# Optimization experiments

Measured on AMD Instinct MI355X. Metric: run time of the kernel, lower is better.

## Reference

```python
import jax, jax.numpy as jnp
import numpy as np

N_TYPES = 4
N_RELS = 8
N, E, IN_DIM, OUT_DIM = 100000, 1600000, 64, 64
SQRT_DK = float(np.sqrt(OUT_DIM))  # num_heads = 1 -> d_k = out_dim


def setup_inputs() -> dict:
    key = jax.random.key(0)
    ks = jax.random.split(key, 12)
    s = 0.05  # keep activations well-scaled (xavier-ish)
    h = jax.random.normal(ks[0], (N, IN_DIM), jnp.float32)
    node_type = jax.random.randint(ks[1], (N,), 0, N_TYPES, jnp.int32)
    src = jax.random.randint(ks[2], (E,), 0, N, jnp.int32)
    dst = jax.random.randint(ks[3], (E,), 0, N, jnp.int32)
    etype = jax.random.randint(ks[4], (E,), 0, N_RELS, jnp.int32)
    k_lin = jax.random.normal(ks[5], (N_TYPES, IN_DIM, OUT_DIM), jnp.float32) * s
    q_lin = jax.random.normal(ks[6], (N_TYPES, IN_DIM, OUT_DIM), jnp.float32) * s
    v_lin = jax.random.normal(ks[7], (N_TYPES, IN_DIM, OUT_DIM), jnp.float32) * s
    a_lin = jax.random.normal(ks[8], (N_TYPES, OUT_DIM, OUT_DIM), jnp.float32) * s
    rel_att = jax.random.normal(ks[9], (N_RELS, OUT_DIM, OUT_DIM), jnp.float32) * s
    rel_msg = jax.random.normal(ks[10], (N_RELS, OUT_DIM, OUT_DIM), jnp.float32) * s
    rel_pri = jnp.ones((N_RELS,), jnp.float32)
    skip = jnp.ones((N_TYPES,), jnp.float32)
    return dict(h=h, node_type=node_type, src=src, dst=dst, etype=etype,
                k_lin=k_lin, q_lin=q_lin, v_lin=v_lin, a_lin=a_lin,
                rel_att=rel_att, rel_msg=rel_msg, rel_pri=rel_pri, skip=skip)


def _typed_matmul(x, W, node_type):
    # rgnn_relational_matmul_no_scatter_gather_list: per-node-type GEMM.
    # Small fixed loop over node types (4), masked accumulate.
    out = jnp.zeros((x.shape[0], W.shape[-1]), x.dtype)
    for t in range(W.shape[0]):
        out = out + jnp.where((node_type == t)[:, None], x @ W[t], 0.0)
    return out


def reference(h, node_type, src, dst, etype, k_lin, q_lin, v_lin, a_lin,
              rel_att, rel_msg, rel_pri, skip):
    # per-node-type K/Q/V projections (num_heads==1, d_k==out_dim)
    k = _typed_matmul(h, k_lin, node_type)  # [N, d_k]
    q = _typed_matmul(h, q_lin, node_type)  # [N, d_k]
    v = _typed_matmul(h, v_lin, node_type)  # [N, d_k]

    # q @ relation_att, computed per relation for ALL nodes then gathered per edge
    # (avoids materializing [E, d_k, d_k] relation weights per edge)
    qW = jnp.einsum('nd,rde->rne', q, rel_att)  # [R, N, d_k]
    t_edge = qW[etype, dst]                      # [E, d_k]  (dst-side product)
    # attention score: <q_dst @ W_att_r, k_src>
    score = jnp.sum(t_edge * k[src], axis=-1)    # [E]

    # edge softmax over incoming edges of each dst, scaled by pri/sqrt(d_k)
    logits = score * (rel_pri / SQRT_DK)[etype]
    m = jax.ops.segment_max(logits, dst, num_segments=N)
    ex = jnp.exp(logits - m[dst])
    den = jax.ops.segment_sum(ex, dst, num_segments=N)
    alpha = ex / jnp.where(den[dst] == 0, 1.0, den[dst])  # [E]

    # message: v_src @ W_msg_r, per relation then gathered per edge
    vW = jnp.einsum('nd,rde->rne', v, rel_msg)   # [R, N, d_k]
    msg = vW[etype, src]                          # [E, d_k]

    # softmax-weighted aggregation to dst nodes
    agg = jax.ops.segment_sum(alpha[:, None] * msg, dst, num_segments=N)  # [N, d_k]

    # output per-node-type GEMM with sigmoid(skip)-scaled a_linears
    W_out = jax.nn.sigmoid(skip)[:, None, None] * a_lin
    return _typed_matmul(agg, W_out, node_type)  # [N, out_dim]
```

## Files before the change

kernel.cpp:

```cpp
#include <hip/hip_runtime.h>
#include <math.h>

#define DIM 64
#define NT 4
#define NR 8

typedef __attribute__((ext_vector_type(8))) short bf16x8;
typedef __attribute__((ext_vector_type(8))) unsigned short u16x8;
typedef __attribute__((ext_vector_type(4))) float f32x4;

__device__ __forceinline__ unsigned short f2bf(float f) {
    unsigned u = __float_as_uint(f);
    return (unsigned short)((u + 0x7FFF + ((u >> 16) & 1)) >> 16);
}
__device__ __forceinline__ float bf2f(unsigned short u) {
    return __uint_as_float((unsigned)u << 16);
}
__device__ __forceinline__ bf16x8 ldb16(const unsigned short* p) {
    return *((const bf16x8*)p);
}

__global__ void type_count(const int* __restrict__ ntype, int* __restrict__ tm, int N) {
    int i = blockIdx.x * blockDim.x + threadIdx.x;
    int t = (i < N) ? ntype[i] : -1;
    int lane = threadIdx.x & 63;
    #pragma unroll
    for (int tt = 0; tt < NT; tt++) {
        unsigned long long m = __ballot(t == tt);
        int c = __popcll(m);
        if (c && lane == (__ffsll((long long)m) - 1)) atomicAdd(&tm[tt], c);
    }
}

__global__ void type_scan(int* __restrict__ tm) {
    if (threadIdx.x == 0 && blockIdx.x == 0) {
        int b = 0;
        for (int t = 0; t < NT; t++) { tm[4 + t] = b; b += ((tm[t] + 63) >> 6) << 6; }
        tm[12] = b;
    }
}

__global__ void type_scatter(const int* __restrict__ ntype, int* __restrict__ tm,
                             int* __restrict__ order, int N) {
    int i = blockIdx.x * blockDim.x + threadIdx.x;
    int t = (i < N) ? ntype[i] : -1;
    int lane = threadIdx.x & 63;
    #pragma unroll
    for (int tt = 0; tt < NT; tt++) {
        unsigned long long m = __ballot(t == tt);
        int c = __popcll(m);
        if (!c) continue;
        int ldr = __ffsll((long long)m) - 1;
        int base = 0;
        if (lane == ldr) base = atomicAdd(&tm[8 + tt], c);
        base = __shfl(base, ldr, 64);
        if (t == tt) {
            int rank = __popcll(m & ((1ull << lane) - 1ull));
            order[tm[4 + tt] + base + rank] = i;
        }
    }
}

__global__ void proj_typed(const float* __restrict__ h, const int* __restrict__ ntype,
                           const int* __restrict__ order, const int* __restrict__ tm,
                           const float* __restrict__ Wk, const float* __restrict__ Wq,
                           const float* __restrict__ Wv,
                           unsigned short* __restrict__ kvbf, unsigned short* __restrict__ qbf,
                           int N) {
    __shared__ float xs[64][68];
    __shared__ float wsm[64][64];
    int t  = threadIdx.x;
    int n0 = blockIdx.x * 64;
    if (n0 >= tm[12]) return;
    int first = order[n0];
    if (first < 0) return;
    int ty = ntype[first];

    #pragma unroll
    for (int i = 0; i < 4; i++) {
        int idx = t + 256 * i;
        int row = idx >> 4, c4 = idx & 15;
        int gn = order[n0 + row];
        float4 xv = make_float4(0.f, 0.f, 0.f, 0.f);
        if (gn >= 0) xv = ((const float4*)(h + (size_t)gn * DIM))[c4];
        ((float4*)&xs[row][0])[c4] = xv;
    }

    const float* Ws[3] = { Wk + (size_t)ty * DIM * DIM,
                           Wq + (size_t)ty * DIM * DIM,
                           Wv + (size_t)ty * DIM * DIM };
    unsigned short* Os[3] = { kvbf, qbf, kvbf + 64 };
    const size_t   st[3] = { 128, 64, 128 };

    int og  = t & 15;
    int ng4 = (t >> 4) * 4;
    int g[4];
    #pragma unroll
    for (int j = 0; j < 4; j++) g[j] = order[n0 + ng4 + j];

    for (int mm = 0; mm < 3; mm++) {
        const float4* wg = (const float4*)Ws[mm];
        float4* wl = (float4*)&wsm[0][0];
        __syncthreads();
        #pragma unroll
        for (int i = 0; i < 4; i++) wl[t + 256 * i] = wg[t + 256 * i];
        __syncthreads();
        float4 a[4];
        #pragma unroll
        for (int j = 0; j < 4; j++) a[j] = make_float4(0.f, 0.f, 0.f, 0.f);
        #pragma unroll 8
        for (int d = 0; d < DIM; d++) {
            float4 wv = ((const float4*)&wsm[d][0])[og];
            #pragma unroll
            for (int j = 0; j < 4; j++) {
                float xx = xs[ng4 + j][d];
                a[j].x = fmaf(xx, wv.x, a[j].x); a[j].y = fmaf(xx, wv.y, a[j].y);
                a[j].z = fmaf(xx, wv.z, a[j].z); a[j].w = fmaf(xx, wv.w, a[j].w);
            }
        }
        unsigned short* ob = Os[mm];
        #pragma unroll
        for (int j = 0; j < 4; j++)
            if (g[j] >= 0)
                ((ushort4*)(ob + (size_t)g[j] * st[mm]))[og] =
                    make_ushort4(f2bf(a[j].x), f2bf(a[j].y), f2bf(a[j].z), f2bf(a[j].w));
    }
}

__global__ void prep_w(const float* __restrict__ A, const float* __restrict__ Mw,
                       unsigned short* __restrict__ At, unsigned short* __restrict__ Mt) {
    int i = blockIdx.x * blockDim.x + threadIdx.x;
    if (i >= NR * DIM * DIM) return;
    int r = i >> 12;
    int idx = i & 4095;
    int n = idx >> 6;
    int k = idx & 63;
    At[i] = f2bf(A[(r << 12) + k * DIM + n]);
    Mt[i] = f2bf(Mw[(r << 12) + k * DIM + n]);
}

__global__ void hist8(const int* __restrict__ dst, const int* __restrict__ et,
                      int* __restrict__ cnt, int E) {
    int e = blockIdx.x * blockDim.x + threadIdx.x;
    if (e < E) atomicAdd(&cnt[dst[e] * NR + et[e]], 1);
}

__global__ void scan1(const int* __restrict__ cnt, int* __restrict__ off,
                      int* __restrict__ bsum, int M) {
    __shared__ int buf[1024];
    int tid = threadIdx.x;
    int i = blockIdx.x * 1024 + tid;
    int x = (i < M) ? cnt[i] : 0;
    buf[tid] = x;
    __syncthreads();
    for (int s = 1; s < 1024; s <<= 1) {
        int t = (tid >= s) ? buf[tid - s] : 0;
        __syncthreads();
        buf[tid] += t;
        __syncthreads();
    }
    if (i < M) off[i] = buf[tid] - x;
    if (tid == 1023) bsum[blockIdx.x] = buf[1023];
}

__global__ void scan2(int* __restrict__ bsum, int nb) {
    __shared__ int buf[1024];
    __shared__ int carry;
    int tid = threadIdx.x;
    if (tid == 0) carry = 0;
    __syncthreads();
    for (int base = 0; base < nb; base += 1024) {
        int i = base + tid;
        int x = (i < nb) ? bsum[i] : 0;
        buf[tid] = x;
        __syncthreads();
        for (int s = 1; s < 1024; s <<= 1) {
            int t = (tid >= s) ? buf[tid - s] : 0;
            __syncthreads();
            buf[tid] += t;
            __syncthreads();
        }
        if (i < nb) bsum[i] = carry + buf[tid] - x;
        __syncthreads();
        if (tid == 1023) carry += buf[1023];
        __syncthreads();
    }
}

__global__ void scan3(int* __restrict__ off, const int* __restrict__ bsum, int M, int E) {
    int i = blockIdx.x * 1024 + threadIdx.x;
    if (i < M) off[i] += bsum[blockIdx.x];
    if (i == 0) off[M] = E;
}

__global__ void scatter8(const int* __restrict__ src, const int* __restrict__ dst,
                         const int* __restrict__ et, const int* __restrict__ off,
                         int* __restrict__ cnt2, int* __restrict__ se, int E) {
    int e = blockIdx.x * blockDim.x + threadIdx.x;
    if (e >= E) return;
    int key = dst[e] * NR + et[e];
    int p = off[key] + atomicAdd(&cnt2[key], 1);
    se[p] = src[e];
}

__global__ void __launch_bounds__(256)
fused_edge(const unsigned short* __restrict__ qbf,
           const unsigned short* __restrict__ kvbf,
           const unsigned short* __restrict__ At,
           const unsigned short* __restrict__ Mt,
           const int* __restrict__ se, const int* __restrict__ off8,
           const float* __restrict__ rel_pri,
           float* __restrict__ agg, int N) {
    __shared__ __align__(16) float qw[4][16][68];
    __shared__ __align__(16) unsigned short pl[4][16][72];
    const int t    = threadIdx.x;
    const int wave = t >> 6;
    const int m    = t & 15;
    const int quad = (t >> 4) & 3;
    const int half = m >> 3;
    const int oct  = m & 7;
    const int n0   = blockIdx.x * 64 + wave * 16;
    if (n0 >= N) return;

    bf16x8 qa0 = {0,0,0,0,0,0,0,0}, qa1 = {0,0,0,0,0,0,0,0};
    {
        const int gn = n0 + m;
        if (gn < N) {
            const unsigned short* qp = qbf + ((size_t)gn << 6) + quad * 8;
            qa0 = *((const bf16x8*)qp);
            qa1 = *((const bf16x8*)(qp + 32));
        }
    }

    int ov[4];
    #pragma unroll
    for (int j = 0; j < 4; j++) {
        const int nj = n0 + quad * 4 + j;
        ov[j] = (m < 9 && nj < N) ? off8[nj * NR + m] : 0;
    }

    f32x4 u0 = {0.f,0.f,0.f,0.f}, u1 = u0, u2 = u0, u3 = u0;
    float d0 = 0.f, d1 = 0.f, d2 = 0.f, d3 = 0.f;

    for (int r = 0; r < NR; r++) {
        const unsigned short* Ar = At + ((size_t)r << 12);
        f32x4 c0 = {0.f,0.f,0.f,0.f}, c1 = c0, c2 = c0, c3 = c0;
        c0 = __builtin_amdgcn_mfma_f32_16x16x32_bf16(qa0, ldb16(Ar + (( 0 + m) << 6)      + quad * 8), c0, 0, 0, 0);
        c1 = __builtin_amdgcn_mfma_f32_16x16x32_bf16(qa0, ldb16(Ar + ((16 + m) << 6)      + quad * 8), c1, 0, 0, 0);
        c2 = __builtin_amdgcn_mfma_f32_16x16x32_bf16(qa0, ldb16(Ar + ((32 + m) << 6)      + quad * 8), c2, 0, 0, 0);
        c3 = __builtin_amdgcn_mfma_f32_16x16x32_bf16(qa0, ldb16(Ar + ((48 + m) << 6)      + quad * 8), c3, 0, 0, 0);
        c0 = __builtin_amdgcn_mfma_f32_16x16x32_bf16(qa1, ldb16(Ar + (( 0 + m) << 6) + 32 + quad * 8), c0, 0, 0, 0);
        c1 = __builtin_amdgcn_mfma_f32_16x16x32_bf16(qa1, ldb16(Ar + ((16 + m) << 6) + 32 + quad * 8), c1, 0, 0, 0);
        c2 = __builtin_amdgcn_mfma_f32_16x16x32_bf16(qa1, ldb16(Ar + ((32 + m) << 6) + 32 + quad * 8), c2, 0, 0, 0);
        c3 = __builtin_amdgcn_mfma_f32_16x16x32_bf16(qa1, ldb16(Ar + ((48 + m) << 6) + 32 + quad * 8), c3, 0, 0, 0);

        #pragma unroll
        for (int reg = 0; reg < 4; reg++) {
            float* qr = &qw[wave][quad * 4 + reg][m];
            qr[ 0] = c0[reg]; qr[16] = c1[reg]; qr[32] = c2[reg]; qr[48] = c3[reg];
        }
        asm volatile("s_waitcnt lgkmcnt(0)" ::: "memory");

        const float pri = rel_pri[r] * 0.125f;
        #pragma unroll
        for (int j = 0; j < 4; j++) {
            const int i0 = __shfl(ov[j], r, 16);
            const int i1 = __shfl(ov[j], r + 1, 16);
            float dd = 0.f;
            float4 pa = make_float4(0.f, 0.f, 0.f, 0.f);
            float4 pb = make_float4(0.f, 0.f, 0.f, 0.f);
            if (i0 < i1) {
                const float4 tva = *((const float4*)&qw[wave][quad * 4 + j][oct * 8]);
                const float4 tvb = *((const float4*)&qw[wave][quad * 4 + j][oct * 8 + 4]);
                auto edge2 = [&](int base) {
                    const int idx  = base + half;
                    const bool val = idx < i1;
                    const int s    = se[val ? idx : i0];
                    const unsigned short* kvp = kvbf + ((size_t)s << 7) + oct * 8;
                    const u16x8 k8 = *((const u16x8*)kvp);
                    const u16x8 v8 = *((const u16x8*)(kvp + 64));
                    float p  = bf2f(k8[0]) * tva.x + bf2f(k8[1]) * tva.y +
                               bf2f(k8[2]) * tva.z + bf2f(k8[3]) * tva.w;
                    float p2 = bf2f(k8[4]) * tvb.x + bf2f(k8[5]) * tvb.y +
                               bf2f(k8[6]) * tvb.z + bf2f(k8[7]) * tvb.w;
                    p += p2;
                    p += __shfl_xor(p, 1, 16);
                    p += __shfl_xor(p, 2, 16);
                    p += __shfl_xor(p, 4, 16);
                    const float e = val ? __expf(p * pri) : 0.f;
                    dd += e;
                    pa.x = fmaf(e, bf2f(v8[0]), pa.x);
                    pa.y = fmaf(e, bf2f(v8[1]), pa.y);
                    pa.z = fmaf(e, bf2f(v8[2]), pa.z);
                    pa.w = fmaf(e, bf2f(v8[3]), pa.w);
                    pb.x = fmaf(e, bf2f(v8[4]), pb.x);
                    pb.y = fmaf(e, bf2f(v8[5]), pb.y);
                    pb.z = fmaf(e, bf2f(v8[6]), pb.z);
                    pb.w = fmaf(e, bf2f(v8[7]), pb.w);
                };
                int i = i0;
                for (; i + 2 < i1; i += 4) { edge2(i); edge2(i + 2); }
                for (; i < i1; i += 2) edge2(i);
                dd  += __shfl_xor(dd, 8, 16);
                pa.x += __shfl_xor(pa.x, 8, 16);
                pa.y += __shfl_xor(pa.y, 8, 16);
                pa.z += __shfl_xor(pa.z, 8, 16);
                pa.w += __shfl_xor(pa.w, 8, 16);
                pb.x += __shfl_xor(pb.x, 8, 16);
                pb.y += __shfl_xor(pb.y, 8, 16);
                pb.z += __shfl_xor(pb.z, 8, 16);
                pb.w += __shfl_xor(pb.w, 8, 16);
            }
            if (m < 8) {
                u16x8 w;
                w[0] = f2bf(pa.x); w[1] = f2bf(pa.y); w[2] = f2bf(pa.z); w[3] = f2bf(pa.w);
                w[4] = f2bf(pb.x); w[5] = f2bf(pb.y); w[6] = f2bf(pb.z); w[7] = f2bf(pb.w);
                *((u16x8*)&pl[wave][quad * 4 + j][m * 8]) = w;
            }
            if      (j == 0) d0 += dd;
            else if (j == 1) d1 += dd;
            else if (j == 2) d2 += dd;
            else             d3 += dd;
        }
        asm volatile("s_waitcnt lgkmcnt(0)" ::: "memory");

        const unsigned short* Mr = Mt + ((size_t)r << 12);
        const bf16x8 pa0 = *((const bf16x8*)&pl[wave][m][quad * 8]);
        const bf16x8 pa1 = *((const bf16x8*)&pl[wave][m][32 + quad * 8]);
        u0 = __builtin_amdgcn_mfma_f32_16x16x32_bf16(pa0, ldb16(Mr + (( 0 + m) << 6)      + quad * 8), u0, 0, 0, 0);
        u1 = __builtin_amdgcn_mfma_f32_16x16x32_bf16(pa0, ldb16(Mr + ((16 + m) << 6)      + quad * 8), u1, 0, 0, 0);
        u2 = __builtin_amdgcn_mfma_f32_16x16x32_bf16(pa0, ldb16(Mr + ((32 + m) << 6)      + quad * 8), u2, 0, 0, 0);
        u3 = __builtin_amdgcn_mfma_f32_16x16x32_bf16(pa0, ldb16(Mr + ((48 + m) << 6)      + quad * 8), u3, 0, 0, 0);
        u0 = __builtin_amdgcn_mfma_f32_16x16x32_bf16(pa1, ldb16(Mr + (( 0 + m) << 6) + 32 + quad * 8), u0, 0, 0, 0);
        u1 = __builtin_amdgcn_mfma_f32_16x16x32_bf16(pa1, ldb16(Mr + ((16 + m) << 6) + 32 + quad * 8), u1, 0, 0, 0);
        u2 = __builtin_amdgcn_mfma_f32_16x16x32_bf16(pa1, ldb16(Mr + ((32 + m) << 6) + 32 + quad * 8), u2, 0, 0, 0);
        u3 = __builtin_amdgcn_mfma_f32_16x16x32_bf16(pa1, ldb16(Mr + ((48 + m) << 6) + 32 + quad * 8), u3, 0, 0, 0);
        asm volatile("s_waitcnt lgkmcnt(0)" ::: "memory");
    }

    #pragma unroll
    for (int reg = 0; reg < 4; reg++) {
        const int n = n0 + quad * 4 + reg;
        if (n >= N) continue;
        const float dv  = (reg == 0) ? d0 : (reg == 1) ? d1 : (reg == 2) ? d2 : d3;
        const float inv = (dv == 0.f) ? 0.f : 1.f / dv;
        float* rowp = agg + ((size_t)n << 6) + m;
        rowp[ 0] = u0[reg] * inv;
        rowp[16] = u1[reg] * inv;
        rowp[32] = u2[reg] * inv;
        rowp[48] = u3[reg] * inv;
    }
}

__global__ void out_typed(const float* __restrict__ agg, const int* __restrict__ ntype,
                          const int* __restrict__ order, const int* __restrict__ tm,
                          const float* __restrict__ Wa, const float* __restrict__ skip,
                          float* __restrict__ out, int N) {
    __shared__ float xs[64][68];
    __shared__ float wsm[64][64];
    int t  = threadIdx.x;
    int n0 = blockIdx.x * 64;
    if (n0 >= tm[12]) return;
    int first = order[n0];
    if (first < 0) return;
    int ty = ntype[first];
    float sg = 1.f / (1.f + expf(-skip[ty]));

    const float4* wg = (const float4*)(Wa + (size_t)ty * DIM * DIM);
    float4* wl = (float4*)&wsm[0][0];
    #pragma unroll
    for (int i = 0; i < 4; i++) {
        float4 w = wg[t + 256 * i];
        w.x *= sg; w.y *= sg; w.z *= sg; w.w *= sg;
        wl[t + 256 * i] = w;
    }
    #pragma unroll
    for (int i = 0; i < 4; i++) {
        int idx = t + 256 * i;
        int row = idx >> 4, c4 = idx & 15;
        int gn = order[n0 + row];
        float4 xv = make_float4(0.f, 0.f, 0.f, 0.f);
        if (gn >= 0) xv = ((const float4*)(agg + (size_t)gn * DIM))[c4];
        ((float4*)&xs[row][0])[c4] = xv;
    }
    __syncthreads();

    int og  = t & 15;
    int ng4 = (t >> 4) * 4;
    float4 a0 = make_float4(0.f,0.f,0.f,0.f), a1 = a0, a2 = a0, a3 = a0;
    #pragma unroll 8
    for (int d = 0; d < DIM; d++) {
        float4 wv = ((const float4*)&wsm[d][0])[og];
        float x0 = xs[ng4 + 0][d];
        float x1 = xs[ng4 + 1][d];
        float x2 = xs[ng4 + 2][d];
        float x3 = xs[ng4 + 3][d];
        a0.x = fmaf(x0, wv.x, a0.x); a0.y = fmaf(x0, wv.y, a0.y);
        a0.z = fmaf(x0, wv.z, a0.z); a0.w = fmaf(x0, wv.w, a0.w);
        a1.x = fmaf(x1, wv.x, a1.x); a1.y = fmaf(x1, wv.y, a1.y);
        a1.z = fmaf(x1, wv.z, a1.z); a1.w = fmaf(x1, wv.w, a1.w);
        a2.x = fmaf(x2, wv.x, a2.x); a2.y = fmaf(x2, wv.y, a2.y);
        a2.z = fmaf(x2, wv.z, a2.z); a2.w = fmaf(x2, wv.w, a2.w);
        a3.x = fmaf(x3, wv.x, a3.x); a3.y = fmaf(x3, wv.y, a3.y);
        a3.z = fmaf(x3, wv.z, a3.z); a3.w = fmaf(x3, wv.w, a3.w);
    }
    int g0 = order[n0 + ng4 + 0];
    int g1 = order[n0 + ng4 + 1];
    int g2 = order[n0 + ng4 + 2];
    int g3 = order[n0 + ng4 + 3];
    if (g0 >= 0) ((float4*)(out + (size_t)g0 * DIM))[og] = a0;
    if (g1 >= 0) ((float4*)(out + (size_t)g1 * DIM))[og] = a1;
    if (g2 >= 0) ((float4*)(out + (size_t)g2 * DIM))[og] = a2;
    if (g3 >= 0) ((float4*)(out + (size_t)g3 * DIM))[og] = a3;
}

extern "C" void kernel_launch(void* const* d_in, const int* in_sizes, int n_in,
                              void* d_out, int out_size, void* d_ws, size_t ws_size,
                              hipStream_t stream) {
    const float* h       = (const float*)d_in[0];
    const int*   ntype   = (const int*)  d_in[1];
    const int*   src     = (const int*)  d_in[2];
    const int*   dst     = (const int*)  d_in[3];
    const int*   et      = (const int*)  d_in[4];
    const float* k_lin   = (const float*)d_in[5];
    const float* q_lin   = (const float*)d_in[6];
    const float* v_lin   = (const float*)d_in[7];
    const float* a_lin   = (const float*)d_in[8];
    const float* rel_att = (const float*)d_in[9];
    const float* rel_msg = (const float*)d_in[10];
    const float* rel_pri = (const float*)d_in[11];
    const float* skip    = (const float*)d_in[12];

    int N = in_sizes[1];
    int E = in_sizes[2];
    int M = N * NR;
    int ocap = N + NT * 64;

    float* ws = (float*)d_ws;
    size_t o = 0;
    unsigned short* kvbf = (unsigned short*)(ws + o); o += (size_t)N * DIM;
    unsigned short* qbf  = (unsigned short*)(ws + o); o += (size_t)N * DIM / 2;
    float* agg  = ws + o; o += (size_t)N * DIM;
    int* off8   = (int*)(ws + o); o += (size_t)M + 8;
    int* cnt8   = (int*)(ws + o); o += (size_t)M;
    int* cnt28  = (int*)(ws + o); o += (size_t)M;
    int* se     = (int*)(ws + o); o += (size_t)E;
    int* bsum   = (int*)(ws + o); o += 1024;
    int* order  = (int*)(ws + o); o += (size_t)ocap;
    int* tm     = (int*)(ws + o); o += 16;
    unsigned short* At = (unsigned short*)(ws + o); o += (size_t)NR * DIM * DIM / 2;
    unsigned short* Mt = (unsigned short*)(ws + o); o += (size_t)NR * DIM * DIM / 2;

    float* out = (float*)d_out;

    hipMemsetAsync(order, 0xFF, (size_t)ocap * 4, stream);
    hipMemsetAsync(tm, 0, 16 * 4, stream);
    hipMemsetAsync(cnt8, 0, (size_t)2 * M * 4, stream);

    type_count<<<(N + 255) / 256, 256, 0, stream>>>(ntype, tm, N);
    type_scan<<<1, 64, 0, stream>>>(tm);
    type_scatter<<<(N + 255) / 256, 256, 0, stream>>>(ntype, tm, order, N);

    int gridT = (N + NT * 64 + 63) / 64;
    proj_typed<<<gridT, 256, 0, stream>>>(h, ntype, order, tm, k_lin, q_lin, v_lin,
                                          kvbf, qbf, N);

    prep_w<<<(NR * DIM * DIM + 255) / 256, 256, 0, stream>>>(rel_att, rel_msg, At, Mt);

    hist8<<<(E + 255) / 256, 256, 0, stream>>>(dst, et, cnt8, E);
    int nb = (M + 1023) / 1024;
    scan1<<<nb, 1024, 0, stream>>>(cnt8, off8, bsum, M);
    scan2<<<1, 1024, 0, stream>>>(bsum, nb);
    scan3<<<nb, 1024, 0, stream>>>(off8, bsum, M, E);
    scatter8<<<(E + 255) / 256, 256, 0, stream>>>(src, dst, et, off8, cnt28, se, E);

    int nb64 = (N + 63) / 64;
    fused_edge<<<nb64, 256, 0, stream>>>(qbf, kvbf, At, Mt, se, off8,
                                         rel_pri, agg, N);

    out_typed<<<gridT, 256, 0, stream>>>(agg, ntype, order, tm, a_lin, skip, out, N);
}
```

Baseline: 687.7 us.

## Use MFMA for typed projections and remap edge loop to 4 lanes per node

```diff
diff --git a/kernel.cpp b/kernel.cpp
--- a/kernel.cpp
+++ b/kernel.cpp
@@ -61,14 +61,33 @@
     }
 }
 
-__global__ void proj_typed(const float* __restrict__ h, const int* __restrict__ ntype,
-                           const int* __restrict__ order, const int* __restrict__ tm,
-                           const float* __restrict__ Wk, const float* __restrict__ Wq,
-                           const float* __restrict__ Wv,
-                           unsigned short* __restrict__ kvbf, unsigned short* __restrict__ qbf,
-                           int N) {
-    __shared__ float xs[64][68];
-    __shared__ float wsm[64][64];
+__global__ void prep_all(const float* __restrict__ A, const float* __restrict__ Mw,
+                         const float* __restrict__ kl, const float* __restrict__ ql,
+                         const float* __restrict__ vl,
+                         unsigned short* __restrict__ At, unsigned short* __restrict__ Mt,
+                         unsigned short* __restrict__ Wkt, unsigned short* __restrict__ Wqt,
+                         unsigned short* __restrict__ Wvt) {
+    int i = blockIdx.x * blockDim.x + threadIdx.x;
+    if (i >= 28 * DIM * DIM) return;
+    int mat = i >> 12;
+    int idx = i & 4095;
+    int n = idx >> 6;
+    int k = idx & 63;
+    int so = k * DIM + n;
+    if (mat < 8)       At [((size_t)mat << 12) + idx]        = f2bf(A [((size_t)mat << 12) + so]);
+    else if (mat < 16) Mt [((size_t)(mat - 8) << 12) + idx]  = f2bf(Mw[((size_t)(mat - 8) << 12) + so]);
+    else if (mat < 20) Wkt[((size_t)(mat - 16) << 12) + idx] = f2bf(kl[((size_t)(mat - 16) << 12) + so]);
+    else if (mat < 24) Wqt[((size_t)(mat - 20) << 12) + idx] = f2bf(ql[((size_t)(mat - 20) << 12) + so]);
+    else               Wvt[((size_t)(mat - 24) << 12) + idx] = f2bf(vl[((size_t)(mat - 24) << 12) + so]);
+}
+
+__global__ void __launch_bounds__(256)
+proj_mfma(const float* __restrict__ h, const int* __restrict__ ntype,
+          const int* __restrict__ order, const int* __restrict__ tm,
+          const unsigned short* __restrict__ Wkt, const unsigned short* __restrict__ Wqt,
+          const unsigned short* __restrict__ Wvt,
+          unsigned short* __restrict__ kvbf, unsigned short* __restrict__ qbf, int N) {
+    __shared__ __align__(16) unsigned short xs[64][72];
     int t  = threadIdx.x;
     int n0 = blockIdx.x * 64;
     if (n0 >= tm[12]) return;
@@ -83,60 +102,48 @@
         int gn = order[n0 + row];
         float4 xv = make_float4(0.f, 0.f, 0.f, 0.f);
         if (gn >= 0) xv = ((const float4*)(h + (size_t)gn * DIM))[c4];
-        ((float4*)&xs[row][0])[c4] = xv;
-    }
-
-    const float* Ws[3] = { Wk + (size_t)ty * DIM * DIM,
-                           Wq + (size_t)ty * DIM * DIM,
-                           Wv + (size_t)ty * DIM * DIM };
-    unsigned short* Os[3] = { kvbf, qbf, kvbf + 64 };
-    const size_t   st[3] = { 128, 64, 128 };
-
-    int og  = t & 15;
-    int ng4 = (t >> 4) * 4;
+        ushort4 b = make_ushort4(f2bf(xv.x), f2bf(xv.y), f2bf(xv.z), f2bf(xv.w));
+        *((ushort4*)&xs[row][c4 * 4]) = b;
+    }
+    __syncthreads();
+
+    int wave = t >> 6, lane = t & 63;
+    int m = lane & 15, quad = lane >> 4;
+    bf16x8 xa0 = *((const bf16x8*)&xs[wave * 16 + m][quad * 8]);
+    bf16x8 xa1 = *((const bf16x8*)&xs[wave * 16 + m][32 + quad * 8]);
+
     int g[4];
     #pragma unroll
-    for (int j = 0; j < 4; j++) g[j] = order[n0 + ng4 + j];
-
+    for (int reg = 0; reg < 4; reg++) g[reg] = order[n0 + wave * 16 + quad * 4 + reg];
+
+    const unsigned short* Wt[3] = { Wkt + (size_t)ty * 4096,
+                                    Wqt + (size_t)ty * 4096,
+                                    Wvt + (size_t)ty * 4096 };
     for (int mm = 0; mm < 3; mm++) {
-        const float4* wg = (const float4*)Ws[mm];
-        float4* wl = (float4*)&wsm[0][0];
-        __syncthreads();
+        const unsigned short* W = Wt[mm];
+        f32x4 c0 = {0.f,0.f,0.f,0.f}, c1 = c0, c2 = c0, c3 = c0;
+        c0 = __builtin_amdgcn_mfma_f32_16x16x32_bf16(xa0, ldb16(W + (( 0 + m) << 6)      + quad * 8), c0, 0, 0, 0);
+        c1 = __builtin_amdgcn_mfma_f32_16x16x32_bf16(xa0, ldb16(W + ((16 + m) << 6)      + quad * 8), c1, 0, 0, 0);
+        c2 = __builtin_amdgcn_mfma_f32_16x16x32_bf16(xa0, ldb16(W + ((32 + m) << 6)      + quad * 8), c2, 0, 0, 0);
+        c3 = __builtin_amdgcn_mfma_f32_16x16x32_bf16(xa0, ldb16(W + ((48 + m) << 6)      + quad * 8), c3, 0, 0, 0);
+        c0 = __builtin_amdgcn_mfma_f32_16x16x32_bf16(xa1, ldb16(W + (( 0 + m) << 6) + 32 + quad * 8), c0, 0, 0, 0);
+        c1 = __builtin_amdgcn_mfma_f32_16x16x32_bf16(xa1, ldb16(W + ((16 + m) << 6) + 32 + quad * 8), c1, 0, 0, 0);
+        c2 = __builtin_amdgcn_mfma_f32_16x16x32_bf16(xa1, ldb16(W + ((32 + m) << 6) + 32 + quad * 8), c2, 0, 0, 0);
+        c3 = __builtin_amdgcn_mfma_f32_16x16x32_bf16(xa1, ldb16(W + ((48 + m) << 6) + 32 + quad * 8), c3, 0, 0, 0);
+
         #pragma unroll
-        for (int i = 0; i < 4; i++) wl[t + 256 * i] = wg[t + 256 * i];
-        __syncthreads();
-        float4 a[4];
-        #pragma unroll
-        for (int j = 0; j < 4; j++) a[j] = make_float4(0.f, 0.f, 0.f, 0.f);
-        #pragma unroll 8
-        for (int d = 0; d < DIM; d++) {
-            float4 wv = ((const float4*)&wsm[d][0])[og];
-            #pragma unroll
-            for (int j = 0; j < 4; j++) {
-                float xx = xs[ng4 + j][d];
-                a[j].x = fmaf(xx, wv.x, a[j].x); a[j].y = fmaf(xx, wv.y, a[j].y);
-                a[j].z = fmaf(xx, wv.z, a[j].z); a[j].w = fmaf(xx, wv.w, a[j].w);
-            }
-        }
-        unsigned short* ob = Os[mm];
-        #pragma unroll
-        for (int j = 0; j < 4; j++)
-            if (g[j] >= 0)
-                ((ushort4*)(ob + (size_t)g[j] * st[mm]))[og] =
-                    make_ushort4(f2bf(a[j].x), f2bf(a[j].y), f2bf(a[j].z), f2bf(a[j].w));
-    }
-}
-
-__global__ void prep_w(const float* __restrict__ A, const float* __restrict__ Mw,
-                       unsigned short* __restrict__ At, unsigned short* __restrict__ Mt) {
-    int i = blockIdx.x * blockDim.x + threadIdx.x;
-    if (i >= NR * DIM * DIM) return;
-    int r = i >> 12;
-    int idx = i & 4095;
-    int n = idx >> 6;
-    int k = idx & 63;
-    At[i] = f2bf(A[(r << 12) + k * DIM + n]);
-    Mt[i] = f2bf(Mw[(r << 12) + k * DIM + n]);
+        for (int reg = 0; reg < 4; reg++) {
+            if (g[reg] < 0) continue;
+            unsigned short* row;
+            if (mm == 1)       row = qbf  + ((size_t)g[reg] << 6) + m;
+            else if (mm == 0)  row = kvbf + ((size_t)g[reg] << 7) + m;
+            else               row = kvbf + ((size_t)g[reg] << 7) + 64 + m;
+            row[ 0] = f2bf(c0[reg]);
+            row[16] = f2bf(c1[reg]);
+            row[32] = f2bf(c2[reg]);
+            row[48] = f2bf(c3[reg]);
+        }
+    }
 }
 
 __global__ void hist8(const int* __restrict__ dst, const int* __restrict__ et,
@@ -211,14 +218,15 @@
            const int* __restrict__ se, const int* __restrict__ off8,
            const float* __restrict__ rel_pri,
            float* __restrict__ agg, int N) {
-    __shared__ __align__(16) float qw[4][16][68];
+    __shared__ __align__(16) unsigned short qwb[4][16][72];
     __shared__ __align__(16) unsigned short pl[4][16][72];
     const int t    = threadIdx.x;
     const int wave = t >> 6;
-    const int m    = t & 15;
-    const int quad = (t >> 4) & 3;
-    const int half = m >> 3;
-    const int oct  = m & 7;
+    const int lane = t & 63;
+    const int m    = lane & 15;
+    const int quad = lane >> 4;
+    const int sg   = lane >> 2;
+    const int ll   = lane & 3;
     const int n0   = blockIdx.x * 64 + wave * 16;
     if (n0 >= N) return;
 
@@ -232,15 +240,14 @@
         }
     }
 
-    int ov[4];
-    #pragma unroll
-    for (int j = 0; j < 4; j++) {
-        const int nj = n0 + quad * 4 + j;
-        ov[j] = (m < 9 && nj < N) ? off8[nj * NR + m] : 0;
-    }
+    const int ob = n0 * NR;
+    const int ov0 = off8[ob + lane];
+    const int ov1 = off8[ob + 64 + lane];
+    const int ov2 = off8[ob + 128];
+    const bool act = (n0 + sg) < N;
 
     f32x4 u0 = {0.f,0.f,0.f,0.f}, u1 = u0, u2 = u0, u3 = u0;
-    float d0 = 0.f, d1 = 0.f, d2 = 0.f, d3 = 0.f;
+    float ddsum = 0.f;
 
     for (int r = 0; r < NR; r++) {
         const unsigned short* Ar = At + ((size_t)r << 12);
@@ -256,72 +263,82 @@
 
         #pragma unroll
         for (int reg = 0; reg < 4; reg++) {
-            float* qr = &qw[wave][quad * 4 + reg][m];
-            qr[ 0] = c0[reg]; qr[16] = c1[reg]; qr[32] = c2[reg]; qr[48] = c3[reg];
+            unsigned short* qr = &qwb[wave][quad * 4 + reg][m];
+            qr[ 0] = f2bf(c0[reg]); qr[16] = f2bf(c1[reg]);
+            qr[32] = f2bf(c2[reg]); qr[48] = f2bf(c3[reg]);
         }
         asm volatile("s_waitcnt lgkmcnt(0)" ::: "memory");
 
+        const int g  = sg * NR + r;
+        const int g1 = g + 1;
+        const int x0a = __shfl(ov0, g, 64);
+        const int x0b = __shfl(ov1, g - 64, 64);
+        int i0 = (g < 64) ? x0a : x0b;
+        const int x1a = __shfl(ov0, g1, 64);
+        const int x1b = __shfl(ov1, g1 - 64, 64);
+        int i1 = (g1 < 64) ? x1a : ((g1 < 128) ? x1b : ov2);
+        if (!act) i1 = i0;
+
         const float pri = rel_pri[r] * 0.125f;
+        float pe[16], po[16];
         #pragma unroll
-        for (int j = 0; j < 4; j++) {
-            const int i0 = __shfl(ov[j], r, 16);
-            const int i1 = __shfl(ov[j], r + 1, 16);
-            float dd = 0.f;
-            float4 pa = make_float4(0.f, 0.f, 0.f, 0.f);
-            float4 pb = make_float4(0.f, 0.f, 0.f, 0.f);
-            if (i0 < i1) {
-                const float4 tva = *((const float4*)&qw[wave][quad * 4 + j][oct * 8]);
-                const float4 tvb = *((const float4*)&qw[wave][quad * 4 + j][oct * 8 + 4]);
-                auto edge2 = [&](int base) {
-                    const int idx  = base + half;
-                    const bool val = idx < i1;
-                    const int s    = se[val ? idx : i0];
-                    const unsigned short* kvp = kvbf + ((size_t)s << 7) + oct * 8;
-                    const u16x8 k8 = *((const u16x8*)kvp);
-                    const u16x8 v8 = *((const u16x8*)(kvp + 64));
-                    float p  = bf2f(k8[0]) * tva.x + bf2f(k8[1]) * tva.y +
-                               bf2f(k8[2]) * tva.z + bf2f(k8[3]) * tva.w;
-                    float p2 = bf2f(k8[4]) * tvb.x + bf2f(k8[5]) * tvb.y +
-                               bf2f(k8[6]) * tvb.z + bf2f(k8[7]) * tvb.w;
-                    p += p2;
-                    p += __shfl_xor(p, 1, 16);
-                    p += __shfl_xor(p, 2, 16);
-                    p += __shfl_xor(p, 4, 16);
-                    const float e = val ? __expf(p * pri) : 0.f;
-                    dd += e;
-                    pa.x = fmaf(e, bf2f(v8[0]), pa.x);
-                    pa.y = fmaf(e, bf2f(v8[1]), pa.y);
-                    pa.z = fmaf(e, bf2f(v8[2]), pa.z);
-                    pa.w = fmaf(e, bf2f(v8[3]), pa.w);
-                    pb.x = fmaf(e, bf2f(v8[4]), pb.x);
-                    pb.y = fmaf(e, bf2f(v8[5]), pb.y);
-                    pb.z = fmaf(e, bf2f(v8[6]), pb.z);
-                    pb.w = fmaf(e, bf2f(v8[7]), pb.w);
-                };
-                int i = i0;
-                for (; i + 2 < i1; i += 4) { edge2(i); edge2(i + 2); }
-                for (; i < i1; i += 2) edge2(i);
-                dd  += __shfl_xor(dd, 8, 16);
-                pa.x += __shfl_xor(pa.x, 8, 16);
-                pa.y += __shfl_xor(pa.y, 8, 16);
-                pa.z += __shfl_xor(pa.z, 8, 16);
-                pa.w += __shfl_xor(pa.w, 8, 16);
-                pb.x += __shfl_xor(pb.x, 8, 16);
-                pb.y += __shfl_xor(pb.y, 8, 16);
-                pb.z += __shfl_xor(pb.z, 8, 16);
-                pb.w += __shfl_xor(pb.w, 8, 16);
+        for (int x = 0; x < 16; x++) { pe[x] = 0.f; po[x] = 0.f; }
+        float dde = 0.f, ddo = 0.f;
+
+        if (i0 < i1) {
+            const u16x8 tq0 = *((const u16x8*)&qwb[wave][sg][ll * 16]);
+            const u16x8 tq1 = *((const u16x8*)&qwb[wave][sg][ll * 16 + 8]);
+            float tq[16];
+            #pragma unroll
+            for (int x = 0; x < 8; x++) { tq[x] = bf2f(tq0[x]); tq[8 + x] = bf2f(tq1[x]); }
+
+            for (int i = i0; i < i1; i += 2) {
+                const int sA = se[i];
+                const bool hB = (i + 1 < i1);
+                const int sB = se[hB ? i + 1 : i];
+                const unsigned short* pA = kvbf + ((size_t)sA << 7) + ll * 16;
+                const unsigned short* pB = kvbf + ((size_t)sB << 7) + ll * 16;
+                const u16x8 kA0 = *((const u16x8*)pA);
+                const u16x8 kA1 = *((const u16x8*)(pA + 8));
+                const u16x8 vA0 = *((const u16x8*)(pA + 64));
+                const u16x8 vA1 = *((const u16x8*)(pA + 72));
+                const u16x8 kB0 = *((const u16x8*)pB);
+                const u16x8 kB1 = *((const u16x8*)(pB + 8));
+                const u16x8 vB0 = *((const u16x8*)(pB + 64));
+                const u16x8 vB1 = *((const u16x8*)(pB + 72));
+                float sa = 0.f, sb = 0.f;
+                #pragma unroll
+                for (int x = 0; x < 8; x++) {
+                    sa = fmaf(bf2f(kA0[x]), tq[x],     sa);
+                    sa = fmaf(bf2f(kA1[x]), tq[8 + x], sa);
+                    sb = fmaf(bf2f(kB0[x]), tq[x],     sb);
+                    sb = fmaf(bf2f(kB1[x]), tq[8 + x], sb);
+                }
+                sa += __shfl_xor(sa, 1, 4);
+                sa += __shfl_xor(sa, 2, 4);
+                sb += __shfl_xor(sb, 1, 4);
+                sb += __shfl_xor(sb, 2, 4);
+                const float eA = __expf(sa * pri);
+                const float eB = hB ? __expf(sb * pri) : 0.f;
+                dde += eA; ddo += eB;
+                #pragma unroll
+                for (int x = 0; x < 8; x++) {
+                    pe[x]     = fmaf(eA, bf2f(vA0[x]), pe[x]);
+                    pe[8 + x] = fmaf(eA, bf2f(vA1[x]), pe[8 + x]);
+                    po[x]     = fmaf(eB, bf2f(vB0[x]), po[x]);
+                    po[8 + x] = fmaf(eB, bf2f(vB1[x]), po[8 + x]);
+                }
             }
-            if (m < 8) {
-                u16x8 w;
-                w[0] = f2bf(pa.x); w[1] = f2bf(pa.y); w[2] = f2bf(pa.z); w[3] = f2bf(pa.w);
-                w[4] = f2bf(pb.x); w[5] = f2bf(pb.y); w[6] = f2bf(pb.z); w[7] = f2bf(pb.w);
-                *((u16x8*)&pl[wave][quad * 4 + j][m * 8]) = w;
-            }
-            if      (j == 0) d0 += dd;
-            else if (j == 1) d1 += dd;
-            else if (j == 2) d2 += dd;
-            else             d3 += dd;
-        }
+        }
+        u16x8 w0, w1;
+        #pragma unroll
+        for (int x = 0; x < 8; x++) {
+            w0[x] = f2bf(pe[x] + po[x]);
+            w1[x] = f2bf(pe[8 + x] + po[8 + x]);
+        }
+        *((u16x8*)&pl[wave][sg][ll * 16])     = w0;
+        *((u16x8*)&pl[wave][sg][ll * 16 + 8]) = w1;
+        ddsum += dde + ddo;
         asm volatile("s_waitcnt lgkmcnt(0)" ::: "memory");
 
         const unsigned short* Mr = Mt + ((size_t)r << 12);
@@ -342,7 +359,7 @@
     for (int reg = 0; reg < 4; reg++) {
         const int n = n0 + quad * 4 + reg;
         if (n >= N) continue;
-        const float dv  = (reg == 0) ? d0 : (reg == 1) ? d1 : (reg == 2) ? d2 : d3;
+        const float dv  = __shfl(ddsum, (quad * 4 + reg) << 2, 64);
         const float inv = (dv == 0.f) ? 0.f : 1.f / dv;
         float* rowp = agg + ((size_t)n << 6) + m;
         rowp[ 0] = u0[reg] * inv;
@@ -441,15 +458,18 @@
     unsigned short* kvbf = (unsigned short*)(ws + o); o += (size_t)N * DIM;
     unsigned short* qbf  = (unsigned short*)(ws + o); o += (size_t)N * DIM / 2;
     float* agg  = ws + o; o += (size_t)N * DIM;
-    int* off8   = (int*)(ws + o); o += (size_t)M + 8;
+    int* off8   = (int*)(ws + o); o += (size_t)M + 1024;
     int* cnt8   = (int*)(ws + o); o += (size_t)M;
     int* cnt28  = (int*)(ws + o); o += (size_t)M;
     int* se     = (int*)(ws + o); o += (size_t)E;
     int* bsum   = (int*)(ws + o); o += 1024;
     int* order  = (int*)(ws + o); o += (size_t)ocap;
     int* tm     = (int*)(ws + o); o += 16;
-    unsigned short* At = (unsigned short*)(ws + o); o += (size_t)NR * DIM * DIM / 2;
-    unsigned short* Mt = (unsigned short*)(ws + o); o += (size_t)NR * DIM * DIM / 2;
+    unsigned short* At  = (unsigned short*)(ws + o); o += (size_t)NR * DIM * DIM / 2;
+    unsigned short* Mt  = (unsigned short*)(ws + o); o += (size_t)NR * DIM * DIM / 2;
+    unsigned short* Wkt = (unsigned short*)(ws + o); o += (size_t)NT * DIM * DIM / 2;
+    unsigned short* Wqt = (unsigned short*)(ws + o); o += (size_t)NT * DIM * DIM / 2;
+    unsigned short* Wvt = (unsigned short*)(ws + o); o += (size_t)NT * DIM * DIM / 2;
 
     float* out = (float*)d_out;
 
@@ -461,11 +481,12 @@
     type_scan<<<1, 64, 0, stream>>>(tm);
     type_scatter<<<(N + 255) / 256, 256, 0, stream>>>(ntype, tm, order, N);
 
+    prep_all<<<(28 * DIM * DIM + 255) / 256, 256, 0, stream>>>(
+        rel_att, rel_msg, k_lin, q_lin, v_lin, At, Mt, Wkt, Wqt, Wvt);
+
     int gridT = (N + NT * 64 + 63) / 64;
-    proj_typed<<<gridT, 256, 0, stream>>>(h, ntype, order, tm, k_lin, q_lin, v_lin,
-                                          kvbf, qbf, N);
-
-    prep_w<<<(NR * DIM * DIM + 255) / 256, 256, 0, stream>>>(rel_att, rel_msg, At, Mt);
+    proj_mfma<<<gridT, 256, 0, stream>>>(h, ntype, order, tm, Wkt, Wqt, Wvt,
+                                         kvbf, qbf, N);
 
     hist8<<<(E + 255) / 256, 256, 0, stream>>>(dst, et, cnt8, E);
     int nb = (M + 1023) / 1024;
```

Result: faster. 654.7 us (-4.8%).
